# Kernel optimization log

Hardware: AMD Instinct MI355X
Metric: run time of the kernel (lower is better)

## Reference

```python
import jax, jax.numpy as jnp
import numpy as np

B, T, F = 8192, 336, 8
H = 20        # lstm_hidden_size
DENSE = 20
OUT = 1
N_LAYERS = 3


def _param(key, shape, scale):
    return jax.random.uniform(key, shape, jnp.float32, -scale, scale)


def setup_inputs() -> dict:
    key = jax.random.key(0)
    ks = jax.random.split(key, 32)
    s = 1.0 / np.sqrt(H)
    inp = {"x": jax.random.normal(ks[0], (B, T, F), jnp.float32)}
    k = 1
    for l in range(N_LAYERS):
        in_size = F if l == 0 else H
        inp[f"W_ih{l}"] = _param(ks[k], (4 * H, in_size), s); k += 1
        inp[f"W_hh{l}"] = _param(ks[k], (4 * H, H), s); k += 1
        inp[f"b_ih{l}"] = _param(ks[k], (4 * H,), s); k += 1
        inp[f"b_hh{l}"] = _param(ks[k], (4 * H,), s); k += 1
    inp["fc1_w"] = _param(ks[k], (DENSE, H), 1.0 / np.sqrt(H)); k += 1
    inp["fc1_b"] = _param(ks[k], (DENSE,), 1.0 / np.sqrt(H)); k += 1
    inp["fc2_w"] = _param(ks[k], (OUT, DENSE), 1.0 / np.sqrt(DENSE)); k += 1
    inp["fc2_b"] = _param(ks[k], (OUT,), 1.0 / np.sqrt(DENSE)); k += 1
    return inp


def lstm_layer(x, W_ih, W_hh, b_ih, b_hh):
    """PyTorch-convention LSTM over [B, T, in]; returns hidden sequence [B, T, H]."""
    b = x.shape[0]
    # Precompute input contribution for all timesteps in one GEMM: [B, T, 4H]
    xg = jnp.einsum('bti,gi->btg', x, W_ih) + b_ih + b_hh
    W_hh_T = W_hh.T  # [H, 4H]

    def step(carry, xt):
        h, c = carry
        gates = xt + h @ W_hh_T                      # [B, 4H], gate order i,f,g,o
        i, f, g, o = jnp.split(gates, 4, axis=-1)
        i = jax.nn.sigmoid(i)
        f = jax.nn.sigmoid(f)
        g = jnp.tanh(g)
        o = jax.nn.sigmoid(o)
        c = f * c + i * g
        h = o * jnp.tanh(c)
        return (h, c), h

    h0 = jnp.zeros((b, W_hh.shape[1]), x.dtype)
    c0 = jnp.zeros_like(h0)
    _, hs = jax.lax.scan(step, (h0, c0), jnp.swapaxes(xg, 0, 1))  # [T, B, H]
    return jnp.swapaxes(hs, 0, 1)


def reference(x, W_ih0, W_hh0, b_ih0, b_hh0, W_ih1, W_hh1, b_ih1, b_hh1,
              W_ih2, W_hh2, b_ih2, b_hh2, fc1_w, fc1_b, fc2_w, fc2_b):
    layers = [(W_ih0, W_hh0, b_ih0, b_hh0),
              (W_ih1, W_hh1, b_ih1, b_hh1),
              (W_ih2, W_hh2, b_ih2, b_hh2)]
    h = x
    for (wi, wh, bi, bh) in layers:
        h = lstm_layer(h, wi, wh, bi, bh)
    h = h[:, -1, :]                         # last timestep, [B, H]
    # dropout layers are identity at inference
    h = jax.nn.relu(h @ fc1_w.T + fc1_b)    # [B, DENSE]
    return h @ fc2_w.T + fc2_b              # [B, OUT]
```

## Files before the change

### kernel.cpp

```cpp
#include <hip/hip_runtime.h>


#define T_LEN 336
#define NJ 169

typedef _Float16 f16;
typedef _Float16 f16x4 __attribute__((ext_vector_type(4)));
typedef _Float16 f16x8 __attribute__((ext_vector_type(8)));
typedef float f32x4 __attribute__((ext_vector_type(4)));

#define MFMA(a, b, c) __builtin_amdgcn_mfma_f32_16x16x32_f16((a), (b), (c), 0, 0, 0)

#define SWZ1(n, c) ((c) ^ (((n) & 7) << 3))

__device__ __forceinline__ float sigm(float x) {
  return __builtin_amdgcn_rcpf(1.0f + __builtin_amdgcn_exp2f(-1.4426950408889634f * x));
}
__device__ __forceinline__ float tanh_fast(float x) {
  return 2.0f * __builtin_amdgcn_rcpf(1.0f + __builtin_amdgcn_exp2f(-2.8853900817779268f * x)) - 1.0f;
}

#define CELLS5(DI, DF, DG, DO, DL, HV, HL) {                                                \
  { float i_=sigm((DI)[0]), f_=sigm((DF)[0]), g_=tanh_fast((DG)[0]), o_=sigm((DO)[0]);      \
    c0 = f_*c0 + i_*g_; (HV)[0] = (f16)(o_*tanh_fast(c0)); }                                \
  { float i_=sigm((DI)[1]), f_=sigm((DF)[1]), g_=tanh_fast((DG)[1]), o_=sigm((DO)[1]);      \
    c1 = f_*c1 + i_*g_; (HV)[1] = (f16)(o_*tanh_fast(c1)); }                                \
  { float i_=sigm((DI)[2]), f_=sigm((DF)[2]), g_=tanh_fast((DG)[2]), o_=sigm((DO)[2]);      \
    c2 = f_*c2 + i_*g_; (HV)[2] = (f16)(o_*tanh_fast(c2)); }                                \
  { float i_=sigm((DI)[3]), f_=sigm((DF)[3]), g_=tanh_fast((DG)[3]), o_=sigm((DO)[3]);      \
    c3 = f_*c3 + i_*g_; (HV)[3] = (f16)(o_*tanh_fast(c3)); }                                \
  { float i_=sigm((DL)[0]), f_=sigm((DL)[1]), g_=tanh_fast((DL)[2]), o_=sigm((DL)[3]);      \
    cL = f_*cL + i_*g_; (HL) = (f16)(o_*tanh_fast(cL)); } }

#define MIDSTEP(SRC, DSELF, DPUB) {                                                         \
  const f16* s_ = (SRC);                                                                    \
  f16x8 ba = *(const f16x8*)&s_[n * 64 + SWZ1(n, q * 8)];                                   \
  f16x8 bb = *(const f16x8*)&s_[n * 64 + SWZ1(n, 32 + q * 8)];                              \
  f32x4 di = MFMA(Fb0, bb, MFMA(Fa0, ba, Bi));                                              \
  f32x4 df = MFMA(Fb1, bb, MFMA(Fa1, ba, Bf));                                              \
  f32x4 dg = MFMA(Fb2, bb, MFMA(Fa2, ba, Bg));                                              \
  f32x4 dn = MFMA(Fb3, bb, MFMA(Fa3, ba, Bo));                                              \
  f32x4 dl = MFMA(Fb4, bb, MFMA(Fa4, ba, BL));                                              \
  f16x4 hv; f16 hl; CELLS5(di, df, dg, dn, dl, hv, hl)                                      \
  f16* ds_ = (DSELF);                                                                       \
  *(f16x4*)&ds_[n * 64 + SWZ1(n, 32 + q * 4)] = hv;                                         \
  ds_[n * 64 + SWZ1(n, 48 + q)] = hl;                                                       \
  f16* dp_ = (DPUB);                                                                        \
  if (dp_) { *(f16x4*)&dp_[n * 64 + SWZ1(n, q * 4)] = hv;                                   \
             dp_[n * 64 + SWZ1(n, 16 + q)] = hl; } }

#define L0STEP(SRC, DSELF, DPUB) {                                                          \
  const f16* s_ = (SRC);                                                                    \
  f16x8 b0 = *(const f16x8*)&s_[n * 64 + SWZ1(n, q * 8)];                                   \
  f32x4 di = MFMA(Fa0, b0, Bi), df = MFMA(Fa1, b0, Bf), dg = MFMA(Fa2, b0, Bg),             \
        dn = MFMA(Fa3, b0, Bo), dl = MFMA(Fa4, b0, BL);                                     \
  f16x4 hv; f16 hl; CELLS5(di, df, dg, dn, dl, hv, hl)                                      \
  f16* ds_ = (DSELF);                                                                       \
  *(f16x4*)&ds_[n * 64 + SWZ1(n, 8 + q * 4)] = hv;                                          \
  ds_[n * 64 + SWZ1(n, 24 + q)] = hl;                                                       \
  f16* dp_ = (DPUB);                                                                        \
  *(f16x4*)&dp_[n * 64 + SWZ1(n, q * 4)] = hv;                                              \
  dp_[n * 64 + SWZ1(n, 16 + q)] = hl; }

__global__ __launch_bounds__(192, 2) void lstm3_ws_kernel(
    const float* __restrict__ x,
    const float* __restrict__ Wih0, const float* __restrict__ Whh0,
    const float* __restrict__ bih0, const float* __restrict__ bhh0,
    const float* __restrict__ Wih1, const float* __restrict__ Whh1,
    const float* __restrict__ bih1, const float* __restrict__ bhh1,
    const float* __restrict__ Wih2, const float* __restrict__ Whh2,
    const float* __restrict__ bih2, const float* __restrict__ bhh2,
    const float* __restrict__ fc1w, const float* __restrict__ fc1b,
    const float* __restrict__ fc2w, const float* __restrict__ fc2b,
    float* __restrict__ out)
{
  __shared__ __align__(16) f16 zT0[2][16 * 64];
  __shared__ __align__(16) f16 zT1[2][2][16 * 64];
  __shared__ __align__(16) f16 zT2[2][2][16 * 64];
  __shared__ __align__(16) float pbuf[64];

  const int tid  = threadIdx.x;
  const int w    = tid >> 6;
  const int lane = tid & 63;
  const int n = lane & 15;
  const int q = lane >> 4;

  {
    f16x8 zer;
#pragma unroll
    for (int j = 0; j < 8; ++j) zer[j] = (f16)0.f;
    for (int i = tid; i < 256; i += 192) ((f16x8*)&zT0[0][0])[i] = zer;
    for (int i = tid; i < 512; i += 192) ((f16x8*)&zT1[0][0][0])[i] = zer;
    for (int i = tid; i < 512; i += 192) ((f16x8*)&zT2[0][0][0])[i] = zer;
  }
  __syncthreads();

  auto rowmap = [](int T, int m) { return T < 4 ? T * 20 + m : (m & 3) * 20 + 16 + (m >> 2); };

  f16x8 Fa0{}, Fa1{}, Fa2{}, Fa3{}, Fa4{};
  f16x8 Fb0{}, Fb1{}, Fb2{}, Fb3{}, Fb4{};
  f32x4 Bi{}, Bf{}, Bg{}, Bo{}, BL{};
  float c0 = 0.f, c1 = 0.f, c2 = 0.f, c3 = 0.f, cL = 0.f;

  if (w == 0) {
    auto gA0 = [&](int T) {
      int row = rowmap(T, n);
      f16x8 r;
#pragma unroll
      for (int j = 0; j < 8; ++j) {
        int k = q * 8 + j;
        float v = (k < 8) ? Wih0[row * 8 + k] : (k < 28 ? Whh0[row * 20 + k - 8] : 0.f);
        r[j] = (f16)v;
      }
      return r;
    };
    Fa0 = gA0(0); Fa1 = gA0(1); Fa2 = gA0(2); Fa3 = gA0(3); Fa4 = gA0(4);
    auto gB = [&](int T) {
      f32x4 r;
#pragma unroll
      for (int j = 0; j < 4; ++j) { int row = rowmap(T, q * 4 + j); r[j] = bih0[row] + bhh0[row]; }
      return r;
    };
    Bi = gB(0); Bf = gB(1); Bg = gB(2); Bo = gB(3); BL = gB(4);
  } else {
    const float* Wi = (w == 1) ? Wih1 : Wih2;
    const float* Wh = (w == 1) ? Whh1 : Whh2;
    const float* bi = (w == 1) ? bih1 : bih2;
    const float* bh = (w == 1) ? bhh1 : bhh2;
    auto gA = [&](int T, int c) {
      int row = rowmap(T, n);
      const float* W = c ? Wh : Wi;
      f16x8 r;
#pragma unroll
      for (int j = 0; j < 8; ++j) {
        int k = q * 8 + j;
        r[j] = (f16)((k < 20) ? W[row * 20 + k] : 0.f);
      }
      return r;
    };
    Fa0 = gA(0, 0); Fb0 = gA(0, 1);
    Fa1 = gA(1, 0); Fb1 = gA(1, 1);
    Fa2 = gA(2, 0); Fb2 = gA(2, 1);
    Fa3 = gA(3, 0); Fb3 = gA(3, 1);
    Fa4 = gA(4, 0); Fb4 = gA(4, 1);
    auto gB = [&](int T) {
      f32x4 r;
#pragma unroll
      for (int j = 0; j < 4; ++j) { int row = rowmap(T, q * 4 + j); r[j] = bi[row] + bh[row]; }
      return r;
    };
    Bi = gB(0); Bf = gB(1); Bg = gB(2); Bo = gB(3); BL = gB(4);
  }

  const float* xb = x + (size_t)(blockIdx.x * 16 + n) * (T_LEN * 8) + 4 * q;
  f32x4 xA{}, xB{};
  if (w == 0) {
    xA = *(const f32x4*)(xb);
    xB = *(const f32x4*)(xb + 16);
  }

#pragma unroll 1
  for (int j = 0; j <= NJ; ++j) {
    asm volatile("" ::: "memory");
    const int wp = j & 1, rp = wp ^ 1;
    if (w == 0) {
      if (j <= 167) {
        f16x4 xh;
        xh[0] = (f16)xA[0]; xh[1] = (f16)xA[1]; xh[2] = (f16)xA[2]; xh[3] = (f16)xA[3];
        *(f16x4*)&zT0[q >> 1][n * 64 + SWZ1(n, 4 * (q & 1))] = xh;
        xA = xB;
        int pn = j + 2; if (pn > 167) pn = 167;
        xB = *(const f32x4*)(xb + (size_t)pn * 16);
        L0STEP(&zT0[0][0], &zT0[1][0], &zT1[wp][0][0])
        L0STEP(&zT0[1][0], &zT0[0][0], &zT1[wp][1][0])
      }
    } else if (w == 1) {
      if (j >= 1 && j <= 168) {
        MIDSTEP(&zT1[rp][0][0], &zT1[rp][1][0], &zT2[wp][0][0])
        MIDSTEP(&zT1[rp][1][0], &zT1[wp][0][0], &zT2[wp][1][0])
      }
    } else {
      if (j >= 2) {
        MIDSTEP(&zT2[rp][0][0], &zT2[rp][1][0], (f16*)nullptr)
        MIDSTEP(&zT2[rp][1][0], &zT2[wp][0][0], (f16*)nullptr)
      }
    }
    asm volatile("s_waitcnt lgkmcnt(0)\n\ts_barrier" ::: "memory");
  }

  if (w == 2) {
    const f16* hb = &zT2[1][0][0];
    f16x4 hv0 = *(const f16x4*)&hb[n * 64 + SWZ1(n, 32)];
    f16x4 hv1 = *(const f16x4*)&hb[n * 64 + SWZ1(n, 36)];
    f16x4 hv2 = *(const f16x4*)&hb[n * 64 + SWZ1(n, 40)];
    f16x4 hv3 = *(const f16x4*)&hb[n * 64 + SWZ1(n, 44)];
    f16x4 hv4 = *(const f16x4*)&hb[n * 64 + SWZ1(n, 48)];
    float p = 0.f;
#pragma unroll
    for (int i = 0; i < 5; ++i) {
      int d = q * 5 + i;
      const float* wr = fc1w + d * 20;
      float s = fc1b[d]
        + wr[0]  * (float)hv0[0] + wr[1]  * (float)hv0[1] + wr[2]  * (float)hv0[2] + wr[3]  * (float)hv0[3]
        + wr[4]  * (float)hv1[0] + wr[5]  * (float)hv1[1] + wr[6]  * (float)hv1[2] + wr[7]  * (float)hv1[3]
        + wr[8]  * (float)hv2[0] + wr[9]  * (float)hv2[1] + wr[10] * (float)hv2[2] + wr[11] * (float)hv2[3]
        + wr[12] * (float)hv3[0] + wr[13] * (float)hv3[1] + wr[14] * (float)hv3[2] + wr[15] * (float)hv3[3]
        + wr[16] * (float)hv4[0] + wr[17] * (float)hv4[1] + wr[18] * (float)hv4[2] + wr[19] * (float)hv4[3];
      p += fc2w[d] * fmaxf(s, 0.f);
    }
    pbuf[n * 4 + q] = p;
    if (q == 0) {
      f32x4 pv = *(const f32x4*)&pbuf[n * 4];
      out[blockIdx.x * 16 + n] = pv[0] + pv[1] + pv[2] + pv[3] + fc2b[0];
    }
  }
}

extern "C" void kernel_launch(void* const* d_in, const int* in_sizes, int n_in,
                              void* d_out, int out_size, void* d_ws, size_t ws_size,
                              hipStream_t stream) {
  const float* x    = (const float*)d_in[0];
  const float* Wih0 = (const float*)d_in[1];
  const float* Whh0 = (const float*)d_in[2];
  const float* bih0 = (const float*)d_in[3];
  const float* bhh0 = (const float*)d_in[4];
  const float* Wih1 = (const float*)d_in[5];
  const float* Whh1 = (const float*)d_in[6];
  const float* bih1 = (const float*)d_in[7];
  const float* bhh1 = (const float*)d_in[8];
  const float* Wih2 = (const float*)d_in[9];
  const float* Whh2 = (const float*)d_in[10];
  const float* bih2 = (const float*)d_in[11];
  const float* bhh2 = (const float*)d_in[12];
  const float* fc1w = (const float*)d_in[13];
  const float* fc1b = (const float*)d_in[14];
  const float* fc2w = (const float*)d_in[15];
  const float* fc2b = (const float*)d_in[16];
  float* out = (float*)d_out;

  hipLaunchKernelGGL(lstm3_ws_kernel, dim3(8192 / 16), dim3(192), 0, stream,
                     x, Wih0, Whh0, bih0, bhh0,
                     Wih1, Whh1, bih1, bhh1,
                     Wih2, Whh2, bih2, bhh2,
                     fc1w, fc1b, fc2w, fc2b, out);
}
```

Measured before the change: 415.2 us.

## Process four timesteps per barrier in wavefront-pipelined 3-layer LSTM

```diff
diff --git a/kernel.cpp b/kernel.cpp
--- a/kernel.cpp
+++ b/kernel.cpp
@@ -2,7 +2,7 @@
 
 
 #define T_LEN 336
-#define NJ 169
+#define NJ 85
 
 typedef _Float16 f16;
 typedef _Float16 f16x4 __attribute__((ext_vector_type(4)));
@@ -32,33 +32,29 @@
   { float i_=sigm((DL)[0]), f_=sigm((DL)[1]), g_=tanh_fast((DL)[2]), o_=sigm((DL)[3]);      \
     cL = f_*cL + i_*g_; (HL) = (f16)(o_*tanh_fast(cL)); } }
 
-#define MIDSTEP(SRC, DSELF, DPUB) {                                                         \
-  const f16* s_ = (SRC);                                                                    \
-  f16x8 ba = *(const f16x8*)&s_[n * 64 + SWZ1(n, q * 8)];                                   \
-  f16x8 bb = *(const f16x8*)&s_[n * 64 + SWZ1(n, 32 + q * 8)];                              \
-  f32x4 di = MFMA(Fb0, bb, MFMA(Fa0, ba, Bi));                                              \
-  f32x4 df = MFMA(Fb1, bb, MFMA(Fa1, ba, Bf));                                              \
-  f32x4 dg = MFMA(Fb2, bb, MFMA(Fa2, ba, Bg));                                              \
-  f32x4 dn = MFMA(Fb3, bb, MFMA(Fa3, ba, Bo));                                              \
-  f32x4 dl = MFMA(Fb4, bb, MFMA(Fa4, ba, BL));                                              \
+#define MSTEP(BA, SRC, SELF, PUB) {                                                         \
+  f16x8 bb = *(const f16x8*)&(SRC)[n * 64 + SWZ1(n, 32 + q * 8)];                           \
+  f32x4 di = MFMA(Fb0, bb, MFMA(Fa0, (BA), Bi));                                            \
+  f32x4 df = MFMA(Fb1, bb, MFMA(Fa1, (BA), Bf));                                            \
+  f32x4 dg = MFMA(Fb2, bb, MFMA(Fa2, (BA), Bg));                                            \
+  f32x4 dn = MFMA(Fb3, bb, MFMA(Fa3, (BA), Bo));                                            \
+  f32x4 dl = MFMA(Fb4, bb, MFMA(Fa4, (BA), BL));                                            \
   f16x4 hv; f16 hl; CELLS5(di, df, dg, dn, dl, hv, hl)                                      \
-  f16* ds_ = (DSELF);                                                                       \
+  f16* ds_ = (SELF);                                                                        \
   *(f16x4*)&ds_[n * 64 + SWZ1(n, 32 + q * 4)] = hv;                                         \
   ds_[n * 64 + SWZ1(n, 48 + q)] = hl;                                                       \
-  f16* dp_ = (DPUB);                                                                        \
+  f16* dp_ = (PUB);                                                                         \
   if (dp_) { *(f16x4*)&dp_[n * 64 + SWZ1(n, q * 4)] = hv;                                   \
              dp_[n * 64 + SWZ1(n, 16 + q)] = hl; } }
 
-#define L0STEP(SRC, DSELF, DPUB) {                                                          \
-  const f16* s_ = (SRC);                                                                    \
-  f16x8 b0 = *(const f16x8*)&s_[n * 64 + SWZ1(n, q * 8)];                                   \
+#define L0S(S, D, PUB) {                                                                    \
+  f16x8 b0 = *(const f16x8*)&zT0[S][n * 64 + SWZ1(n, q * 8)];                               \
   f32x4 di = MFMA(Fa0, b0, Bi), df = MFMA(Fa1, b0, Bf), dg = MFMA(Fa2, b0, Bg),             \
         dn = MFMA(Fa3, b0, Bo), dl = MFMA(Fa4, b0, BL);                                     \
   f16x4 hv; f16 hl; CELLS5(di, df, dg, dn, dl, hv, hl)                                      \
-  f16* ds_ = (DSELF);                                                                       \
-  *(f16x4*)&ds_[n * 64 + SWZ1(n, 8 + q * 4)] = hv;                                          \
-  ds_[n * 64 + SWZ1(n, 24 + q)] = hl;                                                       \
-  f16* dp_ = (DPUB);                                                                        \
+  *(f16x4*)&zT0[D][n * 64 + SWZ1(n, 8 + q * 4)] = hv;                                       \
+  zT0[D][n * 64 + SWZ1(n, 24 + q)] = hl;                                                    \
+  f16* dp_ = (PUB);                                                                         \
   *(f16x4*)&dp_[n * 64 + SWZ1(n, q * 4)] = hv;                                              \
   dp_[n * 64 + SWZ1(n, 16 + q)] = hl; }
 
@@ -74,9 +70,9 @@
     const float* __restrict__ fc2w, const float* __restrict__ fc2b,
     float* __restrict__ out)
 {
-  __shared__ __align__(16) f16 zT0[2][16 * 64];
-  __shared__ __align__(16) f16 zT1[2][2][16 * 64];
-  __shared__ __align__(16) f16 zT2[2][2][16 * 64];
+  __shared__ __align__(16) f16 zT0[4][16 * 64];
+  __shared__ __align__(16) f16 zT1[2][4][16 * 64];
+  __shared__ __align__(16) f16 zT2[2][4][16 * 64];
   __shared__ __align__(16) float pbuf[64];
 
   const int tid  = threadIdx.x;
@@ -89,9 +85,9 @@
     f16x8 zer;
 #pragma unroll
     for (int j = 0; j < 8; ++j) zer[j] = (f16)0.f;
-    for (int i = tid; i < 256; i += 192) ((f16x8*)&zT0[0][0])[i] = zer;
-    for (int i = tid; i < 512; i += 192) ((f16x8*)&zT1[0][0][0])[i] = zer;
-    for (int i = tid; i < 512; i += 192) ((f16x8*)&zT2[0][0][0])[i] = zer;
+    for (int i = tid; i < 512; i += 192)  ((f16x8*)&zT0[0][0])[i] = zer;
+    for (int i = tid; i < 1024; i += 192) ((f16x8*)&zT1[0][0][0])[i] = zer;
+    for (int i = tid; i < 1024; i += 192) ((f16x8*)&zT2[0][0][0])[i] = zer;
   }
   __syncthreads();
 
@@ -162,29 +158,51 @@
 #pragma unroll 1
   for (int j = 0; j <= NJ; ++j) {
     asm volatile("" ::: "memory");
+    __builtin_amdgcn_s_setprio(1);
     const int wp = j & 1, rp = wp ^ 1;
     if (w == 0) {
-      if (j <= 167) {
+      if (j <= 83) {
         f16x4 xh;
         xh[0] = (f16)xA[0]; xh[1] = (f16)xA[1]; xh[2] = (f16)xA[2]; xh[3] = (f16)xA[3];
         *(f16x4*)&zT0[q >> 1][n * 64 + SWZ1(n, 4 * (q & 1))] = xh;
-        xA = xB;
-        int pn = j + 2; if (pn > 167) pn = 167;
-        xB = *(const f32x4*)(xb + (size_t)pn * 16);
-        L0STEP(&zT0[0][0], &zT0[1][0], &zT1[wp][0][0])
-        L0STEP(&zT0[1][0], &zT0[0][0], &zT1[wp][1][0])
+        xh[0] = (f16)xB[0]; xh[1] = (f16)xB[1]; xh[2] = (f16)xB[2]; xh[3] = (f16)xB[3];
+        *(f16x4*)&zT0[2 + (q >> 1)][n * 64 + SWZ1(n, 4 * (q & 1))] = xh;
+        int g = (j + 1 > 83) ? 83 : j + 1;
+        xA = *(const f32x4*)(xb + (size_t)(2 * g) * 16);
+        xB = *(const f32x4*)(xb + (size_t)(2 * g + 1) * 16);
+        f16* p1 = &zT1[wp][0][0];
+        L0S(0, 1, p1 + 0 * 1024)
+        L0S(1, 2, p1 + 1 * 1024)
+        L0S(2, 3, p1 + 2 * 1024)
+        L0S(3, 0, p1 + 3 * 1024)
       }
     } else if (w == 1) {
-      if (j >= 1 && j <= 168) {
-        MIDSTEP(&zT1[rp][0][0], &zT1[rp][1][0], &zT2[wp][0][0])
-        MIDSTEP(&zT1[rp][1][0], &zT1[wp][0][0], &zT2[wp][1][0])
+      if (j >= 1 && j <= 84) {
+        f16* s1 = &zT1[rp][0][0];
+        f16x8 ba0 = *(const f16x8*)&s1[0 * 1024 + n * 64 + SWZ1(n, q * 8)];
+        f16x8 ba1 = *(const f16x8*)&s1[1 * 1024 + n * 64 + SWZ1(n, q * 8)];
+        f16x8 ba2 = *(const f16x8*)&s1[2 * 1024 + n * 64 + SWZ1(n, q * 8)];
+        f16x8 ba3 = *(const f16x8*)&s1[3 * 1024 + n * 64 + SWZ1(n, q * 8)];
+        f16* p2 = &zT2[wp][0][0];
+        MSTEP(ba0, s1 + 0 * 1024, s1 + 1 * 1024, p2 + 0 * 1024)
+        MSTEP(ba1, s1 + 1 * 1024, s1 + 2 * 1024, p2 + 1 * 1024)
+        MSTEP(ba2, s1 + 2 * 1024, s1 + 3 * 1024, p2 + 2 * 1024)
+        MSTEP(ba3, s1 + 3 * 1024, &zT1[wp][0][0], p2 + 3 * 1024)
       }
     } else {
       if (j >= 2) {
-        MIDSTEP(&zT2[rp][0][0], &zT2[rp][1][0], (f16*)nullptr)
-        MIDSTEP(&zT2[rp][1][0], &zT2[wp][0][0], (f16*)nullptr)
+        f16* s2 = &zT2[rp][0][0];
+        f16x8 ca0 = *(const f16x8*)&s2[0 * 1024 + n * 64 + SWZ1(n, q * 8)];
+        f16x8 ca1 = *(const f16x8*)&s2[1 * 1024 + n * 64 + SWZ1(n, q * 8)];
+        f16x8 ca2 = *(const f16x8*)&s2[2 * 1024 + n * 64 + SWZ1(n, q * 8)];
+        f16x8 ca3 = *(const f16x8*)&s2[3 * 1024 + n * 64 + SWZ1(n, q * 8)];
+        MSTEP(ca0, s2 + 0 * 1024, s2 + 1 * 1024, (f16*)nullptr)
+        MSTEP(ca1, s2 + 1 * 1024, s2 + 2 * 1024, (f16*)nullptr)
+        MSTEP(ca2, s2 + 2 * 1024, s2 + 3 * 1024, (f16*)nullptr)
+        MSTEP(ca3, s2 + 3 * 1024, &zT2[wp][0][0], (f16*)nullptr)
       }
     }
+    __builtin_amdgcn_s_setprio(0);
     asm volatile("s_waitcnt lgkmcnt(0)\n\ts_barrier" ::: "memory");
   }
 
```

Result: faster. 396.5 us (-4.5%).
